# Performance work log

Hardware: AMD Instinct MI355X
Metric: run time of the kernel (lower is better)

The kernel has to match this reference:

```python
import jax, jax.numpy as jnp
import numpy as np
from math import sqrt

N = 50000
E = 800000
D_EMB = 512
DK = 64
DV = 64
HEADS = 8


def setup_inputs() -> dict:
    key = jax.random.key(0)
    k1, k2, k3, k4 = jax.random.split(key, 4)
    x = jax.random.normal(k1, (N, D_EMB), dtype=jnp.float32)
    edge_index = jax.random.randint(k2, (2, E), 0, N, dtype=jnp.int64)
    out_qkv = (2 * DK + DV) * HEADS  # 1536
    W_qkv = jax.random.normal(k3, (out_qkv, D_EMB), dtype=jnp.float32) / sqrt(D_EMB)
    b_qkv = jnp.zeros((out_qkv,), dtype=jnp.float32)
    W_ff = jax.random.normal(k4, (D_EMB, DV * HEADS), dtype=jnp.float32) / sqrt(DV * HEADS)
    b_ff = jnp.zeros((D_EMB,), dtype=jnp.float32)
    return {"x": x, "edge_index": edge_index, "W_qkv": W_qkv, "b_qkv": b_qkv,
            "W_ff": W_ff, "b_ff": b_ff}


def _attention_message(Q, K, V, senders, receivers, n_nodes):
    # Q,K: [N, H, dK], V: [N, H, dV]; edge lists: [E]
    scale = 1.0 / sqrt(Q.shape[-1])
    # per-edge scores: [E, H]
    scores = jnp.einsum('ehd,ehd->eh', Q[receivers], K[senders]) * scale
    # segment softmax over incoming edges of each receiver
    smax = jax.ops.segment_max(scores, receivers, num_segments=n_nodes)  # [N, H]
    ex = jnp.exp(scores - smax[receivers])                               # [E, H]
    denom = jax.ops.segment_sum(ex, receivers, num_segments=n_nodes)    # [N, H]
    att = ex / denom[receivers]                                         # [E, H]
    # weighted scatter of V from senders to receivers: [N, H, dV]
    out = jax.ops.segment_sum(att[:, :, None] * V[senders], receivers,
                              num_segments=n_nodes)
    return out, att


def reference(x, edge_index, W_qkv, b_qkv, W_ff, b_ff):
    n_nodes = x.shape[0]
    qkv = x @ W_qkv.T + b_qkv  # [N, (2*dK+dV)*H]
    Q, K, V = jnp.split(qkv, [DK * HEADS, 2 * DK * HEADS], axis=-1)
    Q = Q.reshape(n_nodes, HEADS, DK)
    K = K.reshape(n_nodes, HEADS, DK)
    V = V.reshape(n_nodes, HEADS, DV)
    senders, receivers = edge_index[0], edge_index[1]
    msg, _ = _attention_message(Q, K, V, senders, receivers, n_nodes)
    # aggregate_heads: flatten heads and project to d_Embedding
    out = msg.reshape(n_nodes, HEADS * DV) @ W_ff.T + b_ff
    return out
```

## Files before the change

kernel.cpp:

```cpp
#include <hip/hip_runtime.h>

static constexpr int NN = 50000;
static constexpr int NE = 800000;
static constexpr int DEMB = 512;
static constexpr int QKV_OUT = 1536;

typedef _Float16 half8 __attribute__((ext_vector_type(8)));
typedef float floatx4 __attribute__((ext_vector_type(4)));

#define KQ_SCALE (127.0f / 5.5f)
#define KQ_DEQ   (5.5f / 127.0f)

static constexpr size_t OFF_QH   = 0;
static constexpr size_t OFF_K8   = 51200000;
static constexpr size_t OFF_V8   = 76800000;
static constexpr size_t OFF_MSG  = 102400000;
static constexpr size_t OFF_SRT  = 153600000;
static constexpr size_t OFF_DEG  = 156800000;
static constexpr size_t OFF_OFFA = 157000000;
static constexpr size_t OFF_CUR  = 157200064;
static constexpr size_t OFF_FLAG = 157400064;
static constexpr size_t OFF_WQH  = 157400128;
static constexpr size_t OFF_WFH  = 158972992;

typedef __attribute__((address_space(1))) const void* gas_ptr;
typedef __attribute__((address_space(3))) void* lds_ptr_t;

__device__ __forceinline__ void load_lds16(const void* g, void* l) {
  __builtin_amdgcn_global_load_lds((gas_ptr)g, (lds_ptr_t)l, 16, 0, 0);
}

__global__ __launch_bounds__(256)
void k_cvt(const float* __restrict__ in, _Float16* __restrict__ out, int n8) {
  int i = blockIdx.x * 256 + threadIdx.x;
  if (i < n8) {
    floatx4 a = *(const floatx4*)(in + (size_t)i * 8);
    floatx4 b = *(const floatx4*)(in + (size_t)i * 8 + 4);
    half8 h;
    #pragma unroll
    for (int q = 0; q < 4; ++q) { h[q] = (_Float16)a[q]; h[q + 4] = (_Float16)b[q]; }
    *(half8*)(out + (size_t)i * 8) = h;
  }
}

__global__ __launch_bounds__(64)
void k_detect64(const void* __restrict__ edge, int* __restrict__ flag) {
  if (threadIdx.x == 0) {
    const int* p = (const int*)edge;
    int is64 = 1;
    for (int i = 0; i < 16; ++i) if (p[2 * i + 1] != 0) is64 = 0;
    *flag = is64;
  }
}

__device__ __forceinline__ int edge_at(const void* edge, int row, int e, int is64) {
  if (is64) return (int)((const long long*)edge)[(size_t)row * NE + e];
  return ((const int*)edge)[(size_t)row * NE + e];
}

__global__ __launch_bounds__(256)
void k_histo(const void* __restrict__ edge, const int* __restrict__ flag,
             int* __restrict__ deg) {
  int e = blockIdx.x * 256 + threadIdx.x;
  if (e < NE) {
    int r = edge_at(edge, 1, e, *flag);
    atomicAdd(&deg[r], 1);
  }
}

__global__ __launch_bounds__(1024)
void k_scan(const int* __restrict__ deg, int* __restrict__ off,
            int* __restrict__ cur, int n) {
  __shared__ int sums[1024];
  int tid = threadIdx.x;
  int per = (n + 1023) >> 10;
  int start = tid * per;
  int end = start + per; if (end > n) end = n;
  int s = 0;
  for (int i = start; i < end; ++i) s += deg[i];
  sums[tid] = s;
  __syncthreads();
  for (int d = 1; d < 1024; d <<= 1) {
    int v = (tid >= d) ? sums[tid - d] : 0;
    __syncthreads();
    sums[tid] += v;
    __syncthreads();
  }
  int run = (tid == 0) ? 0 : sums[tid - 1];
  for (int i = start; i < end; ++i) {
    off[i] = run; cur[i] = run; run += deg[i];
  }
  if (tid == 0) off[n] = sums[1023];
}

__global__ __launch_bounds__(256)
void k_scatter(const void* __restrict__ edge, const int* __restrict__ flag,
               int* __restrict__ cur, int* __restrict__ srt) {
  int e = blockIdx.x * 256 + threadIdx.x;
  if (e < NE) {
    int is64 = *flag;
    int r = edge_at(edge, 1, e, is64);
    int s = edge_at(edge, 0, e, is64);
    int pos = atomicAdd(&cur[r], 1);
    srt[pos] = s;
  }
}

template<int MODE>
__global__ __launch_bounds__(256, 2)
void k_gemm256(const _Float16* __restrict__ Ah, const _Float16* __restrict__ Bh,
               const float* __restrict__ bias,
               void* __restrict__ out0, void* __restrict__ out1, void* __restrict__ out2,
               int M, int N, int K, int nxt) {
  __shared__ _Float16 ldsA[2][256 * 32];
  __shared__ _Float16 ldsB[2][128 * 32];
  const int tid = threadIdx.x;

  const int nwg = gridDim.x;
  const int cpx = nwg >> 3;
  const int w = (blockIdx.x & 7) * cpx + (blockIdx.x >> 3);
  const int m0 = (w / nxt) * 256;
  const int n0 = (w % nxt) * 128;

  const int wid = tid >> 6, lane = tid & 63;

  floatx4 acc[4][8];
  #pragma unroll
  for (int m = 0; m < 4; ++m)
    #pragma unroll
    for (int n = 0; n < 8; ++n)
      #pragma unroll
      for (int q = 0; q < 4; ++q) acc[m][n][q] = 0.f;

  const int srow = tid >> 2;
  const int schunk = (tid & 3) ^ ((srow >> 1) & 3);
  int garow[4];
  #pragma unroll
  for (int c = 0; c < 4; ++c) {
    int gr = m0 + c * 64 + srow;
    garow[c] = gr < M ? gr : M - 1;
  }
  const int fr = lane & 15;
  const int fs = lane >> 4;

  const int KT = K >> 5;

  auto STAGE = [&](int tt) {
    const size_t kb = (size_t)(tt << 5) + schunk * 8;
    char* La = (char*)&ldsA[tt & 1][0];
    char* Lb = (char*)&ldsB[tt & 1][0];
    #pragma unroll
    for (int c = 0; c < 4; ++c)
      load_lds16(Ah + (size_t)garow[c] * K + kb, La + c * 4096 + tid * 16);
    #pragma unroll
    for (int c = 0; c < 2; ++c)
      load_lds16(Bh + (size_t)(n0 + c * 64 + srow) * K + kb, Lb + c * 4096 + tid * 16);
  };

  STAGE(0);
  __syncthreads();

  for (int t = 0; t < KT; ++t) {
    if (t + 1 < KT) STAGE(t + 1);
    const _Float16* La = &ldsA[t & 1][0];
    const _Float16* Lb = &ldsB[t & 1][0];
    half8 a[4], b[8];
    #pragma unroll
    for (int m = 0; m < 4; ++m) {
      int R = wid * 64 + m * 16 + fr;
      int s = fs ^ ((R >> 1) & 3);
      a[m] = *(const half8*)(La + R * 32 + s * 8);
    }
    #pragma unroll
    for (int n = 0; n < 8; ++n) {
      int R = n * 16 + fr;
      int s = fs ^ ((R >> 1) & 3);
      b[n] = *(const half8*)(Lb + R * 32 + s * 8);
    }
    __builtin_amdgcn_s_setprio(1);
    #pragma unroll
    for (int m = 0; m < 4; ++m)
      #pragma unroll
      for (int n = 0; n < 8; ++n)
        acc[m][n] = __builtin_amdgcn_mfma_f32_16x16x32_f16(a[m], b[n], acc[m][n], 0, 0, 0);
    __builtin_amdgcn_s_setprio(0);
    __syncthreads();
  }

  const int fq = fs << 2;
  #pragma unroll
  for (int m = 0; m < 4; ++m) {
    #pragma unroll
    for (int n = 0; n < 8; ++n) {
      int gn = n0 + n * 16 + fr;
      float bv = bias[gn];
      #pragma unroll
      for (int q = 0; q < 4; ++q) {
        int gm = m0 + wid * 64 + m * 16 + fq + q;
        if (gm < M) {
          float val = acc[m][n][q] + bv;
          if (MODE == 0) {
            int region = gn >> 9;
            int col = gn & 511;
            size_t idx = (size_t)gm * 512 + col;
            if (region == 0) ((_Float16*)out0)[idx] = (_Float16)val;
            else {
              float s = fminf(fmaxf(val * KQ_SCALE, -127.f), 127.f);
              signed char c = (signed char)__float2int_rn(s);
              if (region == 1) ((signed char*)out1)[idx] = c;
              else             ((signed char*)out2)[idx] = c;
            }
          } else {
            ((float*)out0)[(size_t)gm * N + gn] = val;
          }
        }
      }
    }
  }
}

__global__ __launch_bounds__(256)
void k_attn(const _Float16* __restrict__ Qh, const signed char* __restrict__ K8,
            const signed char* __restrict__ V8, const int* __restrict__ off,
            const int* __restrict__ srt, _Float16* __restrict__ msg) {
  int r = blockIdx.x * 4 + (threadIdx.x >> 6);
  if (r >= NN) return;
  int lane = threadIdx.x & 63;
  int h = lane >> 3, j = lane & 7;
  int qoff = h * 64 + j * 8;

  half8 qh = *(const half8*)(Qh + (size_t)r * 512 + qoff);
  float q[8];
  #pragma unroll
  for (int i = 0; i < 8; ++i) q[i] = (float)qh[i] * 0.125f * KQ_DEQ;

  float denom = 0.f;
  float acc[8];
  #pragma unroll
  for (int i = 0; i < 8; ++i) acc[i] = 0.f;

  int e0 = off[r], e1 = off[r + 1];
  if (e1 <= e0) {
    half8 z = {};
    *(half8*)(msg + (size_t)r * 512 + qoff) = z;
    return;
  }

  auto gload = [&](uint2& k8, uint2& v8, int s) {
    k8 = *(const uint2*)(K8 + (size_t)s * 512 + qoff);
    v8 = *(const uint2*)(V8 + (size_t)s * 512 + qoff);
  };
  auto consume = [&](uint2 k8, uint2 v8) {
    int xw = (int)k8.x, yw = (int)k8.y;
    float p = 0.f;
    p += q[0] * (float)((xw << 24) >> 24);
    p += q[1] * (float)((xw << 16) >> 24);
    p += q[2] * (float)((xw << 8) >> 24);
    p += q[3] * (float)(xw >> 24);
    p += q[4] * (float)((yw << 24) >> 24);
    p += q[5] * (float)((yw << 16) >> 24);
    p += q[6] * (float)((yw << 8) >> 24);
    p += q[7] * (float)(yw >> 24);
    p += __shfl_xor(p, 1);
    p += __shfl_xor(p, 2);
    p += __shfl_xor(p, 4);
    float w = __expf(p);
    denom += w;
    int vx = (int)v8.x, vy = (int)v8.y;
    acc[0] += w * (float)((vx << 24) >> 24);
    acc[1] += w * (float)((vx << 16) >> 24);
    acc[2] += w * (float)((vx << 8) >> 24);
    acc[3] += w * (float)(vx >> 24);
    acc[4] += w * (float)((vy << 24) >> 24);
    acc[5] += w * (float)((vy << 16) >> 24);
    acc[6] += w * (float)((vy << 8) >> 24);
    acc[7] += w * (float)(vy >> 24);
  };
  auto sidx = [&](int e) { return srt[e < e1 ? e : e1 - 1]; };

  uint2 kb0, kb1, kb2, kb3, vb0, vb1, vb2, vb3;
  gload(kb0, vb0, sidx(e0));
  gload(kb1, vb1, sidx(e0 + 1));
  gload(kb2, vb2, sidx(e0 + 2));
  gload(kb3, vb3, sidx(e0 + 3));
  int sn0 = sidx(e0 + 4), sn1 = sidx(e0 + 5), sn2 = sidx(e0 + 6), sn3 = sidx(e0 + 7);

  int e = e0;
  for (; e + 4 <= e1; e += 4) {
    consume(kb0, vb0); gload(kb0, vb0, sn0);
    consume(kb1, vb1); gload(kb1, vb1, sn1);
    consume(kb2, vb2); gload(kb2, vb2, sn2);
    consume(kb3, vb3); gload(kb3, vb3, sn3);
    sn0 = sidx(e + 8); sn1 = sidx(e + 9); sn2 = sidx(e + 10); sn3 = sidx(e + 11);
  }
  int rem = e1 - e;
  if (rem > 0) consume(kb0, vb0);
  if (rem > 1) consume(kb1, vb1);
  if (rem > 2) consume(kb2, vb2);

  float inv = KQ_DEQ / denom;
  half8 oh;
  #pragma unroll
  for (int i = 0; i < 8; ++i) oh[i] = (_Float16)(acc[i] * inv);
  *(half8*)(msg + (size_t)r * 512 + qoff) = oh;
}

extern "C" void kernel_launch(void* const* d_in, const int* in_sizes, int n_in,
                              void* d_out, int out_size, void* d_ws, size_t ws_size,
                              hipStream_t stream) {
  const float* x     = (const float*)d_in[0];
  const void*  edge  = d_in[1];
  const float* W_qkv = (const float*)d_in[2];
  const float* b_qkv = (const float*)d_in[3];
  const float* W_ff  = (const float*)d_in[4];
  const float* b_ff  = (const float*)d_in[5];
  float* out = (float*)d_out;

  char* ws = (char*)d_ws;
  _Float16* Qh = (_Float16*)(ws + OFF_QH);
  signed char* K8 = (signed char*)(ws + OFF_K8);
  signed char* V8 = (signed char*)(ws + OFF_V8);
  _Float16* msgb = (_Float16*)(ws + OFF_MSG);
  _Float16* xh   = (_Float16*)(ws + OFF_MSG);
  int* srt  = (int*)(ws + OFF_SRT);
  int* deg  = (int*)(ws + OFF_DEG);
  int* offa = (int*)(ws + OFF_OFFA);
  int* cur  = (int*)(ws + OFF_CUR);
  int* flag = (int*)(ws + OFF_FLAG);
  _Float16* wqh = (_Float16*)(ws + OFF_WQH);
  _Float16* wfh = (_Float16*)(ws + OFF_WFH);

  hipMemsetAsync(deg, 0, NN * sizeof(int), stream);
  k_detect64<<<1, 64, 0, stream>>>(edge, flag);

  k_cvt<<<(NN * DEMB / 8 + 255) / 256, 256, 0, stream>>>(x, xh, NN * DEMB / 8);
  k_cvt<<<(QKV_OUT * DEMB / 8 + 255) / 256, 256, 0, stream>>>(W_qkv, wqh, QKV_OUT * DEMB / 8);
  k_cvt<<<(DEMB * DEMB / 8 + 255) / 256, 256, 0, stream>>>(W_ff, wfh, DEMB * DEMB / 8);

  k_gemm256<0><<<2352, 256, 0, stream>>>(
      xh, wqh, b_qkv, Qh, K8, V8, NN, QKV_OUT, DEMB, 12);

  k_histo<<<(NE + 255) / 256, 256, 0, stream>>>(edge, flag, deg);
  k_scan<<<1, 1024, 0, stream>>>(deg, offa, cur, NN);
  k_scatter<<<(NE + 255) / 256, 256, 0, stream>>>(edge, flag, cur, srt);

  k_attn<<<(NN + 3) / 4, 256, 0, stream>>>(Qh, K8, V8, offa, srt, msgb);

  k_gemm256<1><<<784, 256, 0, stream>>>(
      msgb, wfh, b_ff, out, nullptr, nullptr, NN, DEMB, DEMB, 4);
}
```

Baseline: 573.6 us.

## Interleave int8 K/V per node, keep weights in LDS, fuse histogram into GEMM

The QKV GEMM now writes K and V into one interleaved int8 buffer, so the attention kernel fetches each sender's K and V slice with a single 16-byte load instead of two 8-byte loads. The GEMM is restructured into 512-thread blocks with 512-row tiles. The whole 128x512 weight tile is loaded into LDS once, and A fragments are read straight from global memory with register double-buffering, which removes the per-k-step barriers. The degree histogram runs as extra blocks of the QKV GEMM launch, saving a kernel launch and letting it overlap. The trade-offs are a 128 KB LDS footprint that limits occupancy and uncached global A loads, which may raise memory latency in the GEMM.

After: 542.8 us. 5.4% less time.

```diff
diff --git a/kernel.cpp b/kernel.cpp
--- a/kernel.cpp
+++ b/kernel.cpp
@@ -12,8 +12,7 @@
 #define KQ_DEQ   (5.5f / 127.0f)
 
 static constexpr size_t OFF_QH   = 0;
-static constexpr size_t OFF_K8   = 51200000;
-static constexpr size_t OFF_V8   = 76800000;
+static constexpr size_t OFF_KV8  = 51200000;
 static constexpr size_t OFF_MSG  = 102400000;
 static constexpr size_t OFF_SRT  = 153600000;
 static constexpr size_t OFF_DEG  = 156800000;
@@ -56,16 +55,6 @@
 __device__ __forceinline__ int edge_at(const void* edge, int row, int e, int is64) {
   if (is64) return (int)((const long long*)edge)[(size_t)row * NE + e];
   return ((const int*)edge)[(size_t)row * NE + e];
-}
-
-__global__ __launch_bounds__(256)
-void k_histo(const void* __restrict__ edge, const int* __restrict__ flag,
-             int* __restrict__ deg) {
-  int e = blockIdx.x * 256 + threadIdx.x;
-  if (e < NE) {
-    int r = edge_at(edge, 1, e, *flag);
-    atomicAdd(&deg[r], 1);
-  }
 }
 
 __global__ __launch_bounds__(1024)
@@ -107,22 +96,41 @@
 }
 
 template<int MODE>
-__global__ __launch_bounds__(256, 2)
-void k_gemm256(const _Float16* __restrict__ Ah, const _Float16* __restrict__ Bh,
-               const float* __restrict__ bias,
-               void* __restrict__ out0, void* __restrict__ out1, void* __restrict__ out2,
-               int M, int N, int K, int nxt) {
-  __shared__ _Float16 ldsA[2][256 * 32];
-  __shared__ _Float16 ldsB[2][128 * 32];
+__global__ __launch_bounds__(512, 2)
+void k_gemmB(const _Float16* __restrict__ Ah, const _Float16* __restrict__ Bh,
+             const float* __restrict__ bias,
+             void* __restrict__ out0, void* __restrict__ out1,
+             const void* __restrict__ edge, const int* __restrict__ flag,
+             int* __restrict__ deg,
+             int M, int N, int K, int nxt, int gemmBlocks) {
+  __shared__ _Float16 Bs[128 * 512];
   const int tid = threadIdx.x;
 
-  const int nwg = gridDim.x;
-  const int cpx = nwg >> 3;
+  if (MODE == 0 && blockIdx.x >= gemmBlocks) {
+    int e = (blockIdx.x - gemmBlocks) * 512 + tid;
+    if (e < NE) {
+      int r = edge_at(edge, 1, e, *flag);
+      atomicAdd(&deg[r], 1);
+    }
+    return;
+  }
+
+  const int cpx = gemmBlocks >> 3;
   const int w = (blockIdx.x & 7) * cpx + (blockIdx.x >> 3);
-  const int m0 = (w / nxt) * 256;
+  const int m0 = (w / nxt) * 512;
   const int n0 = (w % nxt) * 128;
 
   const int wid = tid >> 6, lane = tid & 63;
+  const int fr = lane & 15;
+  const int fs = lane >> 4;
+
+  #pragma unroll
+  for (int it = 0; it < 16; ++it) {
+    int L = it * 512 + tid;
+    int row = L >> 6, sc = L & 63;
+    int c = sc ^ (row & 7);
+    load_lds16(Bh + (size_t)(n0 + row) * K + c * 8, (char*)Bs + (size_t)L * 16);
+  }
 
   floatx4 acc[4][8];
   #pragma unroll
@@ -132,59 +140,40 @@
       #pragma unroll
       for (int q = 0; q < 4; ++q) acc[m][n][q] = 0.f;
 
-  const int srow = tid >> 2;
-  const int schunk = (tid & 3) ^ ((srow >> 1) & 3);
-  int garow[4];
-  #pragma unroll
-  for (int c = 0; c < 4; ++c) {
-    int gr = m0 + c * 64 + srow;
-    garow[c] = gr < M ? gr : M - 1;
-  }
-  const int fr = lane & 15;
-  const int fs = lane >> 4;
-
-  const int KT = K >> 5;
-
-  auto STAGE = [&](int tt) {
-    const size_t kb = (size_t)(tt << 5) + schunk * 8;
-    char* La = (char*)&ldsA[tt & 1][0];
-    char* Lb = (char*)&ldsB[tt & 1][0];
-    #pragma unroll
-    for (int c = 0; c < 4; ++c)
-      load_lds16(Ah + (size_t)garow[c] * K + kb, La + c * 4096 + tid * 16);
-    #pragma unroll
-    for (int c = 0; c < 2; ++c)
-      load_lds16(Bh + (size_t)(n0 + c * 64 + srow) * K + kb, Lb + c * 4096 + tid * 16);
+  int arow[4];
+  #pragma unroll
+  for (int m = 0; m < 4; ++m) {
+    int r = m0 + wid * 64 + m * 16 + fr;
+    arow[m] = r < M ? r : M - 1;
+  }
+
+  __syncthreads();
+
+  auto LDA = [&](half8* dst, int t) {
+    const int k0 = t * 32 + fs * 8;
+    #pragma unroll
+    for (int m = 0; m < 4; ++m)
+      dst[m] = *(const half8*)(Ah + (size_t)arow[m] * K + k0);
   };
 
-  STAGE(0);
-  __syncthreads();
-
-  for (int t = 0; t < KT; ++t) {
-    if (t + 1 < KT) STAGE(t + 1);
-    const _Float16* La = &ldsA[t & 1][0];
-    const _Float16* Lb = &ldsB[t & 1][0];
-    half8 a[4], b[8];
-    #pragma unroll
-    for (int m = 0; m < 4; ++m) {
-      int R = wid * 64 + m * 16 + fr;
-      int s = fs ^ ((R >> 1) & 3);
-      a[m] = *(const half8*)(La + R * 32 + s * 8);
-    }
+  half8 a[4], an[4];
+  LDA(a, 0);
+  for (int t = 0; t < 16; ++t) {
+    if (t + 1 < 16) LDA(an, t + 1);
+    half8 b[8];
     #pragma unroll
     for (int n = 0; n < 8; ++n) {
       int R = n * 16 + fr;
-      int s = fs ^ ((R >> 1) & 3);
-      b[n] = *(const half8*)(Lb + R * 32 + s * 8);
+      int c = (t * 4 + fs) ^ (R & 7);
+      b[n] = *(const half8*)(Bs + R * 512 + c * 8);
     }
-    __builtin_amdgcn_s_setprio(1);
     #pragma unroll
     for (int m = 0; m < 4; ++m)
       #pragma unroll
       for (int n = 0; n < 8; ++n)
         acc[m][n] = __builtin_amdgcn_mfma_f32_16x16x32_f16(a[m], b[n], acc[m][n], 0, 0, 0);
-    __builtin_amdgcn_s_setprio(0);
-    __syncthreads();
+    #pragma unroll
+    for (int m = 0; m < 4; ++m) a[m] = an[m];
   }
 
   const int fq = fs << 2;
@@ -201,14 +190,15 @@
           float val = acc[m][n][q] + bv;
           if (MODE == 0) {
             int region = gn >> 9;
-            int col = gn & 511;
-            size_t idx = (size_t)gm * 512 + col;
-            if (region == 0) ((_Float16*)out0)[idx] = (_Float16)val;
-            else {
+            int d = gn & 511;
+            if (region == 0) {
+              ((_Float16*)out0)[(size_t)gm * 512 + d] = (_Float16)val;
+            } else {
               float s = fminf(fmaxf(val * KQ_SCALE, -127.f), 127.f);
               signed char c = (signed char)__float2int_rn(s);
-              if (region == 1) ((signed char*)out1)[idx] = c;
-              else             ((signed char*)out2)[idx] = c;
+              size_t idx = (size_t)gm * 1024 + ((d >> 3) << 4) + (d & 7)
+                         + (region == 2 ? 8 : 0);
+              ((signed char*)out1)[idx] = c;
             }
           } else {
             ((float*)out0)[(size_t)gm * N + gn] = val;
@@ -220,14 +210,13 @@
 }
 
 __global__ __launch_bounds__(256)
-void k_attn(const _Float16* __restrict__ Qh, const signed char* __restrict__ K8,
-            const signed char* __restrict__ V8, const int* __restrict__ off,
-            const int* __restrict__ srt, _Float16* __restrict__ msg) {
+void k_attn(const _Float16* __restrict__ Qh, const unsigned char* __restrict__ KV8,
+            const int* __restrict__ off, const int* __restrict__ srt,
+            _Float16* __restrict__ msg) {
   int r = blockIdx.x * 4 + (threadIdx.x >> 6);
   if (r >= NN) return;
   int lane = threadIdx.x & 63;
-  int h = lane >> 3, j = lane & 7;
-  int qoff = h * 64 + j * 8;
+  int qoff = lane * 8;
 
   half8 qh = *(const half8*)(Qh + (size_t)r * 512 + qoff);
   float q[8];
@@ -246,12 +235,11 @@
     return;
   }
 
-  auto gload = [&](uint2& k8, uint2& v8, int s) {
-    k8 = *(const uint2*)(K8 + (size_t)s * 512 + qoff);
-    v8 = *(const uint2*)(V8 + (size_t)s * 512 + qoff);
+  auto gload = [&](uint4& kv, int s) {
+    kv = *(const uint4*)(KV8 + (size_t)s * 1024 + lane * 16);
   };
-  auto consume = [&](uint2 k8, uint2 v8) {
-    int xw = (int)k8.x, yw = (int)k8.y;
+  auto consume = [&](uint4 kv) {
+    int xw = (int)kv.x, yw = (int)kv.y;
     float p = 0.f;
     p += q[0] * (float)((xw << 24) >> 24);
     p += q[1] * (float)((xw << 16) >> 24);
@@ -266,7 +254,7 @@
     p += __shfl_xor(p, 4);
     float w = __expf(p);
     denom += w;
-    int vx = (int)v8.x, vy = (int)v8.y;
+    int vx = (int)kv.z, vy = (int)kv.w;
     acc[0] += w * (float)((vx << 24) >> 24);
     acc[1] += w * (float)((vx << 16) >> 24);
     acc[2] += w * (float)((vx << 8) >> 24);
@@ -278,25 +266,25 @@
   };
   auto sidx = [&](int e) { return srt[e < e1 ? e : e1 - 1]; };
 
-  uint2 kb0, kb1, kb2, kb3, vb0, vb1, vb2, vb3;
-  gload(kb0, vb0, sidx(e0));
-  gload(kb1, vb1, sidx(e0 + 1));
-  gload(kb2, vb2, sidx(e0 + 2));
-  gload(kb3, vb3, sidx(e0 + 3));
+  uint4 b0, b1, b2, b3;
+  gload(b0, sidx(e0));
+  gload(b1, sidx(e0 + 1));
+  gload(b2, sidx(e0 + 2));
+  gload(b3, sidx(e0 + 3));
   int sn0 = sidx(e0 + 4), sn1 = sidx(e0 + 5), sn2 = sidx(e0 + 6), sn3 = sidx(e0 + 7);
 
   int e = e0;
   for (; e + 4 <= e1; e += 4) {
-    consume(kb0, vb0); gload(kb0, vb0, sn0);
-    consume(kb1, vb1); gload(kb1, vb1, sn1);
-    consume(kb2, vb2); gload(kb2, vb2, sn2);
-    consume(kb3, vb3); gload(kb3, vb3, sn3);
+    consume(b0); gload(b0, sn0);
+    consume(b1); gload(b1, sn1);
+    consume(b2); gload(b2, sn2);
+    consume(b3); gload(b3, sn3);
     sn0 = sidx(e + 8); sn1 = sidx(e + 9); sn2 = sidx(e + 10); sn3 = sidx(e + 11);
   }
   int rem = e1 - e;
-  if (rem > 0) consume(kb0, vb0);
-  if (rem > 1) consume(kb1, vb1);
-  if (rem > 2) consume(kb2, vb2);
+  if (rem > 0) consume(b0);
+  if (rem > 1) consume(b1);
+  if (rem > 2) consume(b2);
 
   float inv = KQ_DEQ / denom;
   half8 oh;
@@ -318,8 +306,7 @@
 
   char* ws = (char*)d_ws;
   _Float16* Qh = (_Float16*)(ws + OFF_QH);
-  signed char* K8 = (signed char*)(ws + OFF_K8);
-  signed char* V8 = (signed char*)(ws + OFF_V8);
+  unsigned char* KV8 = (unsigned char*)(ws + OFF_KV8);
   _Float16* msgb = (_Float16*)(ws + OFF_MSG);
   _Float16* xh   = (_Float16*)(ws + OFF_MSG);
   int* srt  = (int*)(ws + OFF_SRT);
@@ -337,15 +324,18 @@
   k_cvt<<<(QKV_OUT * DEMB / 8 + 255) / 256, 256, 0, stream>>>(W_qkv, wqh, QKV_OUT * DEMB / 8);
   k_cvt<<<(DEMB * DEMB / 8 + 255) / 256, 256, 0, stream>>>(W_ff, wfh, DEMB * DEMB / 8);
 
-  k_gemm256<0><<<2352, 256, 0, stream>>>(
-      xh, wqh, b_qkv, Qh, K8, V8, NN, QKV_OUT, DEMB, 12);
-
-  k_histo<<<(NE + 255) / 256, 256, 0, stream>>>(edge, flag, deg);
+  const int gemmBlocks = 1176;
+  const int histoBlocks = (NE + 511) / 512;
+  k_gemmB<0><<<gemmBlocks + histoBlocks, 512, 0, stream>>>(
+      xh, wqh, b_qkv, Qh, KV8, edge, flag, deg,
+      NN, QKV_OUT, DEMB, 12, gemmBlocks);
+
   k_scan<<<1, 1024, 0, stream>>>(deg, offa, cur, NN);
   k_scatter<<<(NE + 255) / 256, 256, 0, stream>>>(edge, flag, cur, srt);
 
-  k_attn<<<(NN + 3) / 4, 256, 0, stream>>>(Qh, K8, V8, offa, srt, msgb);
-
-  k_gemm256<1><<<784, 256, 0, stream>>>(
-      msgb, wfh, b_ff, out, nullptr, nullptr, NN, DEMB, DEMB, 4);
-}
+  k_attn<<<(NN + 3) / 4, 256, 0, stream>>>(Qh, KV8, offa, srt, msgb);
+
+  k_gemmB<1><<<392, 512, 0, stream>>>(
+      msgb, wfh, b_ff, out, nullptr, nullptr, nullptr, nullptr,
+      NN, DEMB, DEMB, 4, 392);
+}
```
